# Kernel optimization log

Hardware: AMD Instinct MI355X
Metric: run time of the kernel (lower is better)

Reference implementation:

```python
import jax, jax.numpy as jnp
import numpy as np

THRESHOLD = 0.35      # overlap_thresh
NEGPOS_RATIO = 7
VAR0, VAR1 = 0.1, 0.2  # self.variance


def make_priors():
    # Standard RetinaFace 640x640 anchor grid -> 16800 priors (cx, cy, w, h)
    img = 640
    steps = [8, 16, 32]
    min_sizes = [[16, 32], [64, 128], [256, 512]]
    out = []
    for step, ms in zip(steps, min_sizes):
        f = img // step
        ii, jj = np.meshgrid(np.arange(f), np.arange(f), indexing="ij")
        cx = ((jj + 0.5) * step / img).ravel().astype(np.float32)
        cy = ((ii + 0.5) * step / img).ravel().astype(np.float32)
        for m in ms:
            s = np.full_like(cx, m / img)
            out.append(np.stack([cx, cy, s, s], axis=-1))
    return jnp.asarray(np.concatenate(out, axis=0), dtype=jnp.float32)


def jaccard(a, b):
    # a: [O,4] point-form gt boxes, b: [P,4] point-form priors -> IoU [O,P]
    lt = jnp.maximum(a[:, None, :2], b[None, :, :2])
    rb = jnp.minimum(a[:, None, 2:], b[None, :, 2:])
    wh = jnp.clip(rb - lt, 0.0)
    inter = wh[..., 0] * wh[..., 1]
    area_a = ((a[:, 2] - a[:, 0]) * (a[:, 3] - a[:, 1]))[:, None]
    area_b = ((b[:, 2] - b[:, 0]) * (b[:, 3] - b[:, 1]))[None, :]
    return inter / (area_a + area_b - inter)


def setup_inputs() -> dict:
    key = jax.random.key(0)
    ks = jax.random.split(key, 7)
    B, P, O = 64, 16800, 64
    loc_data = jax.random.normal(ks[0], (B, P, 4), jnp.float32)
    conf_data = jax.random.normal(ks[1], (B, P, 2), jnp.float32)
    landm_data = jax.random.normal(ks[2], (B, P, 10), jnp.float32)
    priors = make_priors()
    # targets: [B, O, 15] = [xmin ymin xmax ymax | 10 landmark coords | label]
    c = jax.random.uniform(ks[3], (B, O, 2), minval=0.15, maxval=0.85)
    wh = jax.random.uniform(ks[4], (B, O, 2), minval=0.05, maxval=0.3)
    boxes = jnp.concatenate([jnp.clip(c - wh / 2, 1e-3, 0.999),
                             jnp.clip(c + wh / 2, 1e-3, 0.999)], axis=-1)
    landms = jax.random.uniform(ks[5], (B, O, 10))
    lab = jnp.where(jax.random.uniform(ks[6], (B, O, 1)) < 0.8, 1.0, -1.0)
    targets = jnp.concatenate([boxes, landms, lab], axis=-1).astype(jnp.float32)
    return {"loc_data": loc_data, "conf_data": conf_data,
            "landm_data": landm_data, "priors": priors, "targets": targets}


def _smooth_l1(x):
    ax = jnp.abs(x)
    return jnp.where(ax < 1.0, 0.5 * ax * ax, ax - 0.5)


def reference(loc_data, conf_data, landm_data, priors, targets):
    B, P, C = conf_data.shape
    O = targets.shape[1]
    priors_pf = jnp.concatenate([priors[:, :2] - priors[:, 2:] * 0.5,
                                 priors[:, :2] + priors[:, 2:] * 0.5], axis=1)

    def match_one(t):
        truths = t[:, :4]
        landms = t[:, 4:14]
        labels = t[:, 14].astype(jnp.int32)
        ov = jaccard(truths, priors_pf)               # [O,P]
        bp_ov = ov.max(axis=1)                         # best prior per truth
        bp_idx = jnp.argmax(ov, axis=1)
        valid = bp_ov >= 0.2                           # RetinaFace gt filter
        bt_ov = ov.max(axis=0)                         # best truth per prior
        bt_idx = jnp.argmax(ov, axis=0)
        # index_fill_(best_prior_idx, 2) for valid gts, ensure best prior kept
        bt_ov = bt_ov.at[bp_idx].set(jnp.where(valid, 2.0, bt_ov[bp_idx]))
        bt_idx = bt_idx.at[bp_idx].set(jnp.arange(O))
        matched = truths[bt_idx]                       # [P,4] point form
        conf = labels[bt_idx]
        conf = jnp.where(bt_ov < THRESHOLD, 0, conf)
        # encode loc target
        g_cxcy = ((matched[:, :2] + matched[:, 2:]) * 0.5 - priors[:, :2]) / (VAR0 * priors[:, 2:])
        g_wh = jnp.log((matched[:, 2:] - matched[:, :2]) / priors[:, 2:]) / VAR1
        loc = jnp.concatenate([g_cxcy, g_wh], axis=1)
        # encode landmark target (5 points)
        ml = landms[bt_idx].reshape(P, 5, 2)
        lm = ((ml - priors[:, None, :2]) / (VAR0 * priors[:, None, 2:])).reshape(P, 10)
        any_valid = jnp.any(valid)                     # early-return branch of match()
        return (jnp.where(any_valid, loc, 0.0),
                jnp.where(any_valid, conf, 0),
                jnp.where(any_valid, lm, 0.0))

    loc_t, conf_t, landm_t = jax.vmap(match_one)(targets)
    loc_t = jax.lax.stop_gradient(loc_t)       # targets built from .data in torch
    landm_t = jax.lax.stop_gradient(landm_t)

    # landmark loss over conf_t > 0
    pos1 = conf_t > 0
    N1 = jnp.maximum(pos1.sum().astype(jnp.float32), 1.0)
    loss_landm = jnp.sum(jnp.where(pos1[..., None], _smooth_l1(landm_data - landm_t), 0.0))

    # localization loss over conf_t != 0 (labels -1 and 1 both positive)
    pos = conf_t != 0
    conf_t1 = jnp.where(pos, 1, conf_t)        # conf_t[pos] = 1 -> values in {0,1}
    loss_l = jnp.sum(jnp.where(pos[..., None], _smooth_l1(loc_data - loc_t), 0.0))

    # hard negative mining
    lse = jax.nn.logsumexp(conf_data, axis=2)                       # [B,P]
    picked = jnp.take_along_axis(conf_data, conf_t1[..., None], axis=2)[..., 0]
    ce_all = lse - picked                                            # per-anchor CE
    rank_score = jnp.where(pos, 0.0, ce_all)
    loss_idx = jnp.argsort(-rank_score, axis=1)
    idx_rank = jnp.argsort(loss_idx, axis=1)
    num_pos = pos.sum(axis=1, keepdims=True)
    num_neg = jnp.minimum(NEGPOS_RATIO * num_pos, P - 1)
    neg = idx_rank < num_neg
    union = pos | neg
    loss_c = jnp.sum(jnp.where(union, ce_all, 0.0))

    N = jnp.maximum(num_pos.sum().astype(jnp.float32), 1.0)
    return loss_l / N, loss_c / N, loss_landm / N1
```

## Files before the change

### kernel.cpp

```cpp
#include <hip/hip_runtime.h>
#include <math.h>

#define B 64
#define P 16800
#define O 64
#define THRESH 0.35f
#define VALID_T 0.2f
#define HB 2048
#define HSHIFT 21
#define MULT 2
#define CHB (MULT * 256)
#define NB2 ((P + CHB - 1) / CHB)
#define KD1B (B * NB2)
#define KB2B (B * O / 4)

__device__ __forceinline__ float smooth_l1(float x) {
    float ax = fabsf(x);
    return ax < 1.f ? 0.5f * ax * ax : ax - 0.5f;
}
__device__ __forceinline__ float lse2(float c0, float c1) {
    float m = fmaxf(c0, c1);
    return m + __logf(__expf(c0 - m) + __expf(c1 - m));
}
__device__ __forceinline__ void iou_upd(float4 t, float area_a,
                                        float px1, float py1, float px2, float py2,
                                        float area_b,
                                        float& bnum, float& bden, int& bio, int o) {
    float w = fmaxf(fminf(t.z, px2) - fmaxf(t.x, px1), 0.f);
    float h = fmaxf(fminf(t.w, py2) - fmaxf(t.y, py1), 0.f);
    float inter = w * h;
    float den = area_a + area_b - inter;
    if (inter * bden > bnum * den) { bnum = inter; bden = den; bio = o; }
}
__device__ __forceinline__ float wave_sum(float v) {
#pragma unroll
    for (int s = 32; s > 0; s >>= 1) v += __shfl_down(v, s, 64);
    return v;
}
__device__ __forceinline__ int wave_sum_i(int v) {
#pragma unroll
    for (int s = 32; s > 0; s >>= 1) v += __shfl_down(v, s, 64);
    return v;
}
__device__ __forceinline__ float wave_min(float v) {
#pragma unroll
    for (int s = 32; s > 0; s >>= 1) v = fminf(v, __shfl_xor(v, s, 64));
    return v;
}
__device__ __forceinline__ float wave_max(float v) {
#pragma unroll
    for (int s = 32; s > 0; s >>= 1) v = fmaxf(v, __shfl_xor(v, s, 64));
    return v;
}
__device__ __forceinline__ int wave_sufscan(int v, int lane) {
#pragma unroll
    for (int s = 1; s < 64; s <<= 1) {
        int o = __shfl_down(v, s, 64);
        if (lane + s < 64) v += o;
    }
    return v;
}

__global__ void __launch_bounds__(256) kMain(
        const float* __restrict__ loc_data, const float* __restrict__ conf_data,
        const float* __restrict__ landm_data, const float* __restrict__ priors,
        const float* __restrict__ targets,
        float* __restrict__ rank, int* __restrict__ hist,
        int* __restrict__ num_pos, float* __restrict__ pos_ce,
        float* __restrict__ gsum, int* __restrict__ np1_tot,
        unsigned long long* __restrict__ bp_final) {
    if (blockIdx.x >= KD1B) {
        int pair = (blockIdx.x - KD1B) * 4 + (threadIdx.x >> 6);
        int lane = threadIdx.x & 63;
        int o = pair & (O - 1);
        int b = pair >> 6;
        const float* tt = &targets[(b * O + o) * 15];
        float tx1 = tt[0], ty1 = tt[1], tx2 = tt[2], ty2 = tt[3];
        float area_a = (tx2 - tx1) * (ty2 - ty1);
        float4 tb = make_float4(tx1, ty1, tx2, ty2);
        float bn = 0.f, bd = 1.f;
        unsigned bp = 0u;
        const int fs[6]   = {80, 80, 40, 40, 20, 20};
        const int ms[6]   = {16, 32, 64, 128, 256, 512};
        const int base[6] = {0, 6400, 12800, 14400, 16000, 16400};
#pragma unroll
        for (int c = 0; c < 6; ++c) {
            int f = fs[c];
            float inv = (float)f;
            float h = (float)ms[c] * (0.5f / 640.f);
            int j0 = (int)floorf((tx1 - h) * inv - 0.5f) - 1; if (j0 < 0) j0 = 0;
            int j1 = (int)ceilf((tx2 + h) * inv - 0.5f) + 1;  if (j1 > f - 1) j1 = f - 1;
            int i0 = (int)floorf((ty1 - h) * inv - 0.5f) - 1; if (i0 < 0) i0 = 0;
            int i1 = (int)ceilf((ty2 + h) * inv - 0.5f) + 1;  if (i1 > f - 1) i1 = f - 1;
            if (j1 < j0 || i1 < i0) continue;
            int nj = j1 - j0 + 1;
            int n = (i1 - i0 + 1) * nj;
            float rcp_nj = 1.0f / (float)nj;
            for (int idx = lane; idx < n; idx += 64) {
                int ii = (int)((float)idx * rcp_nj);
                int jj = idx - ii * nj;
                if (jj < 0) { ii--; jj += nj; } else if (jj >= nj) { ii++; jj -= nj; }
                int p = base[c] + (i0 + ii) * f + (j0 + jj);
                float4 q = ((const float4*)priors)[p];
                float px1 = q.x - q.z * 0.5f, py1 = q.y - q.w * 0.5f;
                float px2 = q.x + q.z * 0.5f, py2 = q.y + q.w * 0.5f;
                float areab = (px2 - px1) * (py2 - py1);
                float w = fmaxf(fminf(tb.z, px2) - fmaxf(tb.x, px1), 0.f);
                float hh = fmaxf(fminf(tb.w, py2) - fmaxf(tb.y, py1), 0.f);
                float inter = w * hh;
                float den = area_a + areab - inter;
                float l = bn * den, r = inter * bd;
                if (r > l) { bn = inter; bd = den; bp = (unsigned)p; }
            }
        }
#pragma unroll
        for (int s = 32; s > 0; s >>= 1) {
            float no = __shfl_xor(bn, s, 64), dd = __shfl_xor(bd, s, 64);
            unsigned po = __shfl_xor(bp, s, 64);
            float l = bn * dd, r = no * bd;
            bool take = (r > l) || (r == l && po < bp);
            if (take) { bn = no; bd = dd; bp = po; }
        }
        if (lane == 0) {
            float iou = bn / bd;
            bp_final[b * O + o] = ((unsigned long long)__float_as_uint(iou) << 32)
                                | (unsigned)(0xFFFFFFFFu - bp);
        }
        return;
    }
    int blk = blockIdx.x % NB2;
    int b = blockIdx.x / NB2;
    int p0 = blk * CHB;
    __shared__ float4 t4[O];
    __shared__ float ta[O], lab[O];
    __shared__ float lm[O][10];
    __shared__ int lhist[HB];
    __shared__ float4 wbb[4];
    __shared__ int alist[O];
    __shared__ int s_cnt;
    __shared__ float wredf[3][4];
    __shared__ int wredi[2][4];
    int tid = threadIdx.x;
    if (tid < O) {
        const float* t = &targets[(b * O + tid) * 15];
        float a0 = t[0], a1 = t[1], a2 = t[2], a3 = t[3];
        t4[tid] = make_float4(a0, a1, a2, a3);
        ta[tid] = (a2 - a0) * (a3 - a1);
        lab[tid] = t[14];
    }
    for (int i = tid; i < O * 10; i += 256)
        lm[i / 10][i % 10] = targets[b * O * 15 + (i / 10) * 15 + 4 + (i % 10)];
    for (int i = tid; i < HB; i += 256) lhist[i] = 0;
    float px1[MULT], py1[MULT], px2[MULT], py2[MULT], areab[MULT];
    float4 pr4[MULT];
    float bnum[MULT], bden[MULT]; int bi[MULT]; bool act[MULT];
    float bx1 = 1e30f, by1 = 1e30f, bx2 = -1e30f, by2 = -1e30f;
#pragma unroll
    for (int mi = 0; mi < MULT; ++mi) {
        int p = p0 + mi * 256 + tid;
        act[mi] = (p < P);
        int pc = act[mi] ? p : (P - 1);
        float4 q = ((const float4*)priors)[pc];
        pr4[mi] = q;
        px1[mi] = q.x - q.z * 0.5f; py1[mi] = q.y - q.w * 0.5f;
        px2[mi] = q.x + q.z * 0.5f; py2[mi] = q.y + q.w * 0.5f;
        areab[mi] = (px2[mi] - px1[mi]) * (py2[mi] - py1[mi]);
        bx1 = fminf(bx1, px1[mi]); by1 = fminf(by1, py1[mi]);
        bx2 = fmaxf(bx2, px2[mi]); by2 = fmaxf(by2, py2[mi]);
        bnum[mi] = 0.f; bden[mi] = 1.f; bi[mi] = 0;
    }
    bx1 = wave_min(bx1); by1 = wave_min(by1);
    bx2 = wave_max(bx2); by2 = wave_max(by2);
    int wid = tid >> 6, lid = tid & 63;
    if (lid == 0) wbb[wid] = make_float4(bx1, by1, bx2, by2);
    __syncthreads();
    if (tid < 64) {
        float ux1 = fminf(fminf(wbb[0].x, wbb[1].x), fminf(wbb[2].x, wbb[3].x));
        float uy1 = fminf(fminf(wbb[0].y, wbb[1].y), fminf(wbb[2].y, wbb[3].y));
        float ux2 = fmaxf(fmaxf(wbb[0].z, wbb[1].z), fmaxf(wbb[2].z, wbb[3].z));
        float uy2 = fmaxf(fmaxf(wbb[0].w, wbb[1].w), fmaxf(wbb[2].w, wbb[3].w));
        float4 t = t4[tid];
        bool pass = (fminf(t.z, ux2) - fmaxf(t.x, ux1) > 0.f) &&
                    (fminf(t.w, uy2) - fmaxf(t.y, uy1) > 0.f);
        unsigned long long mask = __ballot(pass);
        if (tid == 0) s_cnt = __popcll(mask);
        if (pass) {
            int pos = __popcll(mask & ((1ull << tid) - 1ull));
            alist[pos] = tid;
        }
    }
    __syncthreads();
    int cnt = s_cnt;
    for (int li = 0; li < cnt; ++li) {
        int o = alist[li];
        float4 t = t4[o];
        float w0 = fminf(t.z, bx2) - fmaxf(t.x, bx1);
        float h0 = fminf(t.w, by2) - fmaxf(t.y, by1);
        if (w0 <= 0.f || h0 <= 0.f) continue;
        float area_a = ta[o];
#pragma unroll
        for (int mi = 0; mi < MULT; ++mi)
            iou_upd(t, area_a, px1[mi], py1[mi], px2[mi], py2[mi], areab[mi],
                    bnum[mi], bden[mi], bi[mi], o);
    }
    float ll = 0.f, llm = 0.f, cep = 0.f;
    int cp = 0, cp1 = 0;
#pragma unroll
    for (int mi = 0; mi < MULT; ++mi) {
        if (!act[mi]) continue;
        int p = p0 + mi * 256 + tid;
        float best = bnum[mi] / bden[mi];
        int conf = (best >= THRESH) ? (int)lab[bi[mi]] : 0;
        float2 c01 = ((const float2*)conf_data)[b * P + p];
        float c0 = c01.x, c1 = c01.y;
        float lse = lse2(c0, c1);
        bool pos = conf != 0;
        float ce = lse - (pos ? c1 : c0);
        float rv = pos ? 0.f : ce;
        rank[(size_t)b * P + p] = rv;
        atomicAdd(&lhist[__float_as_uint(rv) >> HSHIFT], 1);
        if (pos) {
            cp++; cep += ce;
            int ti = bi[mi];
            float cx = pr4[mi].x, cy = pr4[mi].y, sw = pr4[mi].z, sh = pr4[mi].w;
            float4 t = t4[ti];
            float gx = ((t.x + t.z) * 0.5f - cx) / (0.1f * sw);
            float gy = ((t.y + t.w) * 0.5f - cy) / (0.1f * sh);
            float gw = logf((t.z - t.x) / sw) / 0.2f;
            float gh = logf((t.w - t.y) / sh) / 0.2f;
            const float* ld = &loc_data[(size_t)(b * P + p) * 4];
            ll += smooth_l1(ld[0] - gx) + smooth_l1(ld[1] - gy) +
                  smooth_l1(ld[2] - gw) + smooth_l1(ld[3] - gh);
            if (conf > 0) {
                cp1++;
                const float* lmd = &landm_data[(size_t)(b * P + p) * 10];
                for (int k5 = 0; k5 < 5; ++k5) {
                    float lx = (lm[ti][k5 * 2 + 0] - cx) / (0.1f * sw);
                    float ly = (lm[ti][k5 * 2 + 1] - cy) / (0.1f * sh);
                    llm += smooth_l1(lmd[k5 * 2 + 0] - lx) + smooth_l1(lmd[k5 * 2 + 1] - ly);
                }
            }
        }
    }
    float s_ll = wave_sum(ll), s_llm = wave_sum(llm), s_cep = wave_sum(cep);
    int s_cp = wave_sum_i(cp), s_cp1 = wave_sum_i(cp1);
    if (lid == 0) {
        wredf[0][wid] = s_ll; wredf[1][wid] = s_llm; wredf[2][wid] = s_cep;
        wredi[0][wid] = s_cp; wredi[1][wid] = s_cp1;
    }
    __syncthreads();
    if (tid == 0) {
        float ll_t = wredf[0][0] + wredf[0][1] + wredf[0][2] + wredf[0][3];
        float llm_t = wredf[1][0] + wredf[1][1] + wredf[1][2] + wredf[1][3];
        float cep_t = wredf[2][0] + wredf[2][1] + wredf[2][2] + wredf[2][3];
        int cp_t = wredi[0][0] + wredi[0][1] + wredi[0][2] + wredi[0][3];
        int cp1_t = wredi[1][0] + wredi[1][1] + wredi[1][2] + wredi[1][3];
        if (ll_t != 0.f)  atomicAdd(&gsum[0], ll_t);
        if (llm_t != 0.f) atomicAdd(&gsum[1], llm_t);
        if (cep_t != 0.f) atomicAdd(&pos_ce[b], cep_t);
        if (cp_t)  atomicAdd(&num_pos[b], cp_t);
        if (cp1_t) atomicAdd(np1_tot, cp1_t);
    }
    int* gh = hist + (size_t)b * HB;
#pragma unroll
    for (int i = tid; i < HB; i += 256) {
        int c = lhist[i];
        if (c) atomicAdd(&gh[i], c);
    }
}

__global__ void __launch_bounds__(1024) kTail(
        const float* __restrict__ priors, const float* __restrict__ targets,
        const float* __restrict__ loc_data, const float* __restrict__ conf_data,
        const float* __restrict__ landm_data,
        const unsigned long long* __restrict__ bp_final,
        const float* __restrict__ rank, const int* __restrict__ hist,
        const int* __restrict__ num_pos, const float* __restrict__ pos_ce,
        float* __restrict__ gsum, int* __restrict__ np1_tot, int* __restrict__ np_tot,
        float* __restrict__ lossc_tot, int* __restrict__ done,
        float* __restrict__ out) {
    __shared__ __align__(16) unsigned lrow[P];
    __shared__ float4 t4[O];
    __shared__ float ta[O], lab[O];
    __shared__ int sp[O];
    __shared__ int lh[HB];
    __shared__ int chunkSum[256];
    __shared__ int suf[257];
    __shared__ int waveTot[4];
    __shared__ int hist2[256];
    __shared__ int s_np, s_bin0, s_kk0, s_bin, s_kk;
    __shared__ float wredf[16];
    __shared__ int wredi[16];
    __shared__ float s_sumgt;

    int b = blockIdx.x;
    int tid = threadIdx.x;
    const float* r = rank + (size_t)b * P;
    const float4* r4 = (const float4*)r;
    for (int i = tid; i < P / 4; i += 1024) {
        float4 q = r4[i];
        ((uint4*)lrow)[i] = make_uint4(__float_as_uint(q.x), __float_as_uint(q.y),
                                       __float_as_uint(q.z), __float_as_uint(q.w));
    }
    for (int i = tid; i < HB; i += 1024) lh[i] = hist[(size_t)b * HB + i];
    int p = 0, v = 0;
    if (tid < O) {
        const float* tt = &targets[(b * O + tid) * 15];
        float4 tj = make_float4(tt[0], tt[1], tt[2], tt[3]);
        t4[tid] = tj;
        ta[tid] = (tj.z - tj.x) * (tj.w - tj.y);
        lab[tid] = tt[14];
        unsigned long long kpk = bp_final[b * O + tid];
        p = (int)(0xFFFFFFFFu - (unsigned)(kpk & 0xFFFFFFFFu));
        float iou = __uint_as_float((unsigned)(kpk >> 32));
        v = (iou >= VALID_T) ? 1 : 0;
        sp[tid] = p;
    }
    __syncthreads();
    int dnp = 0, dn1 = 0;
    float dll = 0.f, dllm = 0.f, dce = 0.f;
    if (tid < O) {
        int j = tid;
        bool winner = true;
        for (int jj = j + 1; jj < O; ++jj)
            if (sp[jj] == p) { winner = false; break; }
        if (winner) {
            float4 q = ((const float4*)priors)[p];
            float px1 = q.x - q.z * 0.5f, py1 = q.y - q.w * 0.5f;
            float px2 = q.x + q.z * 0.5f, py2 = q.y + q.w * 0.5f;
            float areab = (px2 - px1) * (py2 - py1);
            float bnum = 0.f, bden = 1.f; int bi = 0;
            for (int o = 0; o < O; ++o)
                iou_upd(t4[o], ta[o], px1, py1, px2, py2, areab, bnum, bden, bi, o);
            float best = bnum / bden;
            float ov_new = v ? 2.0f : best;
            int conf_old = (best >= THRESH) ? (int)lab[bi] : 0;
            int conf_new = (ov_new >= THRESH) ? (int)lab[j] : 0;
            float2 c01 = ((const float2*)conf_data)[b * P + p];
            float c0 = c01.x, c1 = c01.y;
            float lse = lse2(c0, c1);
            bool po = conf_old != 0, pn = conf_new != 0;
            float ceo = lse - (po ? c1 : c0), cen = lse - (pn ? c1 : c0);
            float rvo = po ? 0.f : ceo, rvn = pn ? 0.f : cen;
            if (__float_as_uint(rvo) != __float_as_uint(rvn)) {
                lrow[p] = __float_as_uint(rvn);
                int bo = __float_as_uint(rvo) >> HSHIFT, bn = __float_as_uint(rvn) >> HSHIFT;
                if (bo != bn) { atomicAdd(&lh[bn], 1); atomicAdd(&lh[bo], -1); }
            }
            const float* ld = &loc_data[(size_t)(b * P + p) * 4];
            auto enc_ll = [&](int ti) -> float {
                float4 t = t4[ti];
                float gx = ((t.x + t.z) * 0.5f - q.x) / (0.1f * q.z);
                float gy = ((t.y + t.w) * 0.5f - q.y) / (0.1f * q.w);
                float gw = logf((t.z - t.x) / q.z) / 0.2f;
                float gh = logf((t.w - t.y) / q.w) / 0.2f;
                return smooth_l1(ld[0] - gx) + smooth_l1(ld[1] - gy) +
                       smooth_l1(ld[2] - gw) + smooth_l1(ld[3] - gh);
            };
            if (po) dll -= enc_ll(bi);
            if (pn) dll += enc_ll(j);
            dce = (pn ? cen : 0.f) - (po ? ceo : 0.f);
            dnp = (int)pn - (int)po;
            const float* lmd = &landm_data[(size_t)(b * P + p) * 10];
            auto enc_lm = [&](int ti) -> float {
                const float* lmt = &targets[(b * O + ti) * 15 + 4];
                float sum = 0.f;
                for (int k5 = 0; k5 < 5; ++k5) {
                    float lx = (lmt[k5 * 2 + 0] - q.x) / (0.1f * q.z);
                    float ly = (lmt[k5 * 2 + 1] - q.y) / (0.1f * q.w);
                    sum += smooth_l1(lmd[k5 * 2 + 0] - lx) + smooth_l1(lmd[k5 * 2 + 1] - ly);
                }
                return sum;
            };
            if (conf_old > 0) dllm -= enc_lm(bi);
            if (conf_new > 0) dllm += enc_lm(j);
            dn1 = (int)(conf_new > 0) - (int)(conf_old > 0);
        }
    }
    float pce_reg = 0.f;
    if (tid < 64) {
        float r_ll = wave_sum(dll), r_lm = wave_sum(dllm), r_ce = wave_sum(dce);
        int r_np = wave_sum_i(dnp), r_n1 = wave_sum_i(dn1);
        if (tid == 0) {
            if (r_ll != 0.f) atomicAdd(&gsum[0], r_ll);
            if (r_lm != 0.f) atomicAdd(&gsum[1], r_lm);
            pce_reg = pos_ce[b] + r_ce;
            int np = num_pos[b] + r_np;
            s_np = np;
            atomicAdd(np_tot, np);
            if (r_n1) atomicAdd(np1_tot, r_n1);
        }
    }
    __syncthreads();
    int k = s_np * 7;
    if (k > P - 1) k = P - 1;
    if (tid < 256) {
        int cs = 0;
#pragma unroll
        for (int i = 0; i < HB / 256; ++i) cs += lh[tid * (HB / 256) + i];
        chunkSum[tid] = cs;
    }
    if (tid == 0) { s_bin0 = (k <= 0) ? -1 : 0; s_kk0 = (k <= 0) ? 0 : k; }
    __syncthreads();
    {
        int lane = tid & 63;
        int vv = (tid < 256) ? chunkSum[tid] : 0;
        vv = wave_sufscan(vv, lane);
        if (tid < 256 && lane == 0) waveTot[tid >> 6] = vv;
        __syncthreads();
        if (tid < 256) {
            int after = 0;
            for (int g = (tid >> 6) + 1; g < 4; ++g) after += waveTot[g];
            suf[tid] = vv + after;
            if (tid == 0) suf[256] = 0;
        }
        __syncthreads();
        if (k > 0 && tid < 256) {
            if (suf[tid] >= k && suf[tid + 1] < k) {
                int cum = suf[tid + 1];
                for (int i = HB / 256 - 1; i >= 0; --i) {
                    int hv = lh[tid * (HB / 256) + i];
                    if (cum + hv >= k) { s_bin0 = tid * (HB / 256) + i; s_kk0 = k - cum; break; }
                    cum += hv;
                }
            }
        }
    }
    __syncthreads();
    int bin = s_bin0;
    int kk0 = s_kk0;
    float topk_b = 0.f;
    if (bin >= 0) {
        unsigned lo_bound = ((unsigned)(bin + 1)) << HSHIFT;
        float sumgt = 0.f;
        for (int pp = tid; pp < P; pp += 1024) {
            unsigned u = lrow[pp];
            if (u >= lo_bound) sumgt += __uint_as_float(u);
        }
        float sg = wave_sum(sumgt);
        if ((tid & 63) == 0) wredf[tid >> 6] = sg;
        __syncthreads();
        if (tid == 0) {
            float t = 0.f;
            for (int i = 0; i < 16; ++i) t += wredf[i];
            s_sumgt = t;
        }
        unsigned pref = ((unsigned)bin) << HSHIFT;
        unsigned resolved = 0xFFFFFFFFu << HSHIFT;
        int kk = kk0;
        const int shifts[3] = {13, 5, 0};
        const int nbins[3] = {256, 256, 32};
        for (int pass = 0; pass < 3; ++pass) {
            int sh = shifts[pass], nb = nbins[pass];
            if (tid < nb) hist2[tid] = 0;
            __syncthreads();
            for (int i = tid; i < P / 4; i += 1024) {
                uint4 u4 = ((const uint4*)lrow)[i];
                if ((u4.x & resolved) == pref) atomicAdd(&hist2[(u4.x >> sh) & (nb - 1)], 1);
                if ((u4.y & resolved) == pref) atomicAdd(&hist2[(u4.y >> sh) & (nb - 1)], 1);
                if ((u4.z & resolved) == pref) atomicAdd(&hist2[(u4.z >> sh) & (nb - 1)], 1);
                if ((u4.w & resolved) == pref) atomicAdd(&hist2[(u4.w >> sh) & (nb - 1)], 1);
            }
            __syncthreads();
            int lane = tid & 63;
            int vv = (tid < nb) ? hist2[tid] : 0;
            vv = wave_sufscan(vv, lane);
            if (tid < nb && lane == 0) waveTot[tid >> 6] = vv;
            __syncthreads();
            int ng = (nb + 63) >> 6;
            if (tid < nb) {
                int after = 0;
                for (int g = (tid >> 6) + 1; g < ng; ++g) after += waveTot[g];
                suf[tid] = vv + after;
                if (tid == 0) suf[nb] = 0;
            }
            __syncthreads();
            if (tid < nb) {
                if (suf[tid] >= kk && suf[tid + 1] < kk) { s_bin = tid; s_kk = kk - suf[tid + 1]; }
            }
            __syncthreads();
            pref |= ((unsigned)s_bin) << sh;
            resolved |= (unsigned)(nb - 1) << sh;
            kk = s_kk;
            __syncthreads();
        }
        float tv = __uint_as_float(pref);
        float sumS = 0.f; int cntS = 0;
        for (int pp = tid; pp < P; pp += 1024) {
            unsigned u = lrow[pp];
            if ((u >> HSHIFT) == (unsigned)bin) {
                float val = __uint_as_float(u);
                if (val > tv) { sumS += val; cntS++; }
            }
        }
        float s2 = wave_sum(sumS); int c2 = wave_sum_i(cntS);
        if ((tid & 63) == 0) { wredf[tid >> 6] = s2; wredi[tid >> 6] = c2; }
        __syncthreads();
        if (tid == 0) {
            float st = 0.f; int ct = 0;
            for (int i = 0; i < 16; ++i) { st += wredf[i]; ct += wredi[i]; }
            topk_b = s_sumgt + st + (float)(kk0 - ct) * tv;
        }
    }
    if (tid == 0) {
        atomicAdd(lossc_tot, pce_reg + topk_b);
        __threadfence();
        int old = atomicAdd(done, 1);
        if (old == B - 1) {
            float g0 = atomicAdd(&gsum[0], 0.f);
            float g1 = atomicAdd(&gsum[1], 0.f);
            float lc = atomicAdd(lossc_tot, 0.f);
            int np = atomicAdd(np_tot, 0);
            int n1 = atomicAdd(np1_tot, 0);
            float N = fmaxf((float)np, 1.f);
            float N1 = fmaxf((float)n1, 1.f);
            out[0] = g0 / N;
            out[1] = lc / N;
            out[2] = g1 / N1;
        }
    }
}

extern "C" void kernel_launch(void* const* d_in, const int* in_sizes, int n_in,
                              void* d_out, int out_size, void* d_ws, size_t ws_size,
                              hipStream_t stream) {
    const float* loc_data   = (const float*)d_in[0];
    const float* conf_data  = (const float*)d_in[1];
    const float* landm_data = (const float*)d_in[2];
    const float* priors     = (const float*)d_in[3];
    const float* targets    = (const float*)d_in[4];
    float* out = (float*)d_out;

    char* ws = (char*)d_ws;
    size_t off = 0;
    auto alloc = [&](size_t bytes) -> void* {
        void* pp = ws + off;
        off += (bytes + 255) & ~(size_t)255;
        return pp;
    };
    float* rank     = (float*)alloc((size_t)B * P * 4);
    unsigned long long* bp_final = (unsigned long long*)alloc((size_t)B * O * 8);
    size_t hist_bytes = (size_t)B * HB * 4;
    char* zbase = (char*)alloc(hist_bytes);
    int* hist = (int*)zbase;
    size_t acc_bytes = (size_t)(2 * B * 4 + 64);
    char* acc = (char*)alloc(acc_bytes);
    int*   num_pos      = (int*)acc;
    float* pos_ce       = (float*)(acc + B * 4);
    float* gsum         = (float*)(acc + 2 * B * 4);
    int*   np1_tot      = (int*)(acc + 2 * B * 4 + 8);
    int*   np_tot       = (int*)(acc + 2 * B * 4 + 12);
    float* lossc_tot    = (float*)(acc + 2 * B * 4 + 16);
    int*   done         = (int*)(acc + 2 * B * 4 + 20);
    size_t zlen = (size_t)((acc + acc_bytes) - zbase);

    hipMemsetAsync(zbase, 0, zlen, stream);
    kMain<<<dim3(KD1B + KB2B), dim3(256), 0, stream>>>(loc_data, conf_data, landm_data,
                                                       priors, targets, rank, hist,
                                                       num_pos, pos_ce, gsum, np1_tot,
                                                       bp_final);
    kTail<<<dim3(B), dim3(1024), 0, stream>>>(priors, targets, loc_data, conf_data,
                                              landm_data, bp_final, rank, hist,
                                              num_pos, pos_ce, gsum, np1_tot, np_tot,
                                              lossc_tot, done, out);
}
```

Measured before the change: 165.2 us.

## Prune IoU pairs by area ratio and build rank histogram in tail kernel

Adds an area-ratio bound that skips IoU evaluation for gt/prior pairs whose areas differ enough that IoU cannot reach the match threshold, both at block level and per prior. Moves the per-batch rank histogram construction from kMain (shared plus global atomics) into kTail, which counts from the rank row it already loads into shared memory. This removes the global histogram buffer, its memset and the global atomics, at the cost of extra shared atomics in the single-block-per-batch tail kernel.

```diff
diff --git a/kernel.cpp b/kernel.cpp
--- a/kernel.cpp
+++ b/kernel.cpp
@@ -8,6 +8,7 @@
 #define VALID_T 0.2f
 #define HB 2048
 #define HSHIFT 21
+#define AREA_M 0.34f
 #define MULT 2
 #define CHB (MULT * 256)
 #define NB2 ((P + CHB - 1) / CHB)
@@ -65,7 +66,7 @@
         const float* __restrict__ loc_data, const float* __restrict__ conf_data,
         const float* __restrict__ landm_data, const float* __restrict__ priors,
         const float* __restrict__ targets,
-        float* __restrict__ rank, int* __restrict__ hist,
+        float* __restrict__ rank,
         int* __restrict__ num_pos, float* __restrict__ pos_ce,
         float* __restrict__ gsum, int* __restrict__ np1_tot,
         unsigned long long* __restrict__ bp_final) {
@@ -134,8 +135,8 @@
     __shared__ float4 t4[O];
     __shared__ float ta[O], lab[O];
     __shared__ float lm[O][10];
-    __shared__ int lhist[HB];
     __shared__ float4 wbb[4];
+    __shared__ float2 wab[4];
     __shared__ int alist[O];
     __shared__ int s_cnt;
     __shared__ float wredf[3][4];
@@ -150,11 +151,11 @@
     }
     for (int i = tid; i < O * 10; i += 256)
         lm[i / 10][i % 10] = targets[b * O * 15 + (i / 10) * 15 + 4 + (i % 10)];
-    for (int i = tid; i < HB; i += 256) lhist[i] = 0;
     float px1[MULT], py1[MULT], px2[MULT], py2[MULT], areab[MULT];
     float4 pr4[MULT];
     float bnum[MULT], bden[MULT]; int bi[MULT]; bool act[MULT];
     float bx1 = 1e30f, by1 = 1e30f, bx2 = -1e30f, by2 = -1e30f;
+    float amn = 1e30f, amx = -1e30f;
 #pragma unroll
     for (int mi = 0; mi < MULT; ++mi) {
         int p = p0 + mi * 256 + tid;
@@ -167,21 +168,27 @@
         areab[mi] = (px2[mi] - px1[mi]) * (py2[mi] - py1[mi]);
         bx1 = fminf(bx1, px1[mi]); by1 = fminf(by1, py1[mi]);
         bx2 = fmaxf(bx2, px2[mi]); by2 = fmaxf(by2, py2[mi]);
+        amn = fminf(amn, areab[mi]); amx = fmaxf(amx, areab[mi]);
         bnum[mi] = 0.f; bden[mi] = 1.f; bi[mi] = 0;
     }
     bx1 = wave_min(bx1); by1 = wave_min(by1);
     bx2 = wave_max(bx2); by2 = wave_max(by2);
+    amn = wave_min(amn); amx = wave_max(amx);
     int wid = tid >> 6, lid = tid & 63;
-    if (lid == 0) wbb[wid] = make_float4(bx1, by1, bx2, by2);
+    if (lid == 0) { wbb[wid] = make_float4(bx1, by1, bx2, by2); wab[wid] = make_float2(amn, amx); }
     __syncthreads();
     if (tid < 64) {
         float ux1 = fminf(fminf(wbb[0].x, wbb[1].x), fminf(wbb[2].x, wbb[3].x));
         float uy1 = fminf(fminf(wbb[0].y, wbb[1].y), fminf(wbb[2].y, wbb[3].y));
         float ux2 = fmaxf(fmaxf(wbb[0].z, wbb[1].z), fmaxf(wbb[2].z, wbb[3].z));
         float uy2 = fmaxf(fmaxf(wbb[0].w, wbb[1].w), fmaxf(wbb[2].w, wbb[3].w));
+        float bmn = fminf(fminf(wab[0].x, wab[1].x), fminf(wab[2].x, wab[3].x));
+        float bmx = fmaxf(fmaxf(wab[0].y, wab[1].y), fmaxf(wab[2].y, wab[3].y));
         float4 t = t4[tid];
+        float Aa = ta[tid];
         bool pass = (fminf(t.z, ux2) - fmaxf(t.x, ux1) > 0.f) &&
-                    (fminf(t.w, uy2) - fmaxf(t.y, uy1) > 0.f);
+                    (fminf(t.w, uy2) - fmaxf(t.y, uy1) > 0.f) &&
+                    (Aa >= AREA_M * bmn) && (bmx >= AREA_M * Aa);
         unsigned long long mask = __ballot(pass);
         if (tid == 0) s_cnt = __popcll(mask);
         if (pass) {
@@ -197,11 +204,14 @@
         float w0 = fminf(t.z, bx2) - fmaxf(t.x, bx1);
         float h0 = fminf(t.w, by2) - fmaxf(t.y, by1);
         if (w0 <= 0.f || h0 <= 0.f) continue;
-        float area_a = ta[o];
-#pragma unroll
-        for (int mi = 0; mi < MULT; ++mi)
-            iou_upd(t, area_a, px1[mi], py1[mi], px2[mi], py2[mi], areab[mi],
-                    bnum[mi], bden[mi], bi[mi], o);
+        float Aa = ta[o];
+#pragma unroll
+        for (int mi = 0; mi < MULT; ++mi) {
+            float Ap = areab[mi];
+            if (Aa >= AREA_M * Ap && Ap >= AREA_M * Aa)
+                iou_upd(t, Aa, px1[mi], py1[mi], px2[mi], py2[mi], Ap,
+                        bnum[mi], bden[mi], bi[mi], o);
+        }
     }
     float ll = 0.f, llm = 0.f, cep = 0.f;
     int cp = 0, cp1 = 0;
@@ -218,7 +228,6 @@
         float ce = lse - (pos ? c1 : c0);
         float rv = pos ? 0.f : ce;
         rank[(size_t)b * P + p] = rv;
-        atomicAdd(&lhist[__float_as_uint(rv) >> HSHIFT], 1);
         if (pos) {
             cp++; cep += ce;
             int ti = bi[mi];
@@ -261,12 +270,6 @@
         if (cp_t)  atomicAdd(&num_pos[b], cp_t);
         if (cp1_t) atomicAdd(np1_tot, cp1_t);
     }
-    int* gh = hist + (size_t)b * HB;
-#pragma unroll
-    for (int i = tid; i < HB; i += 256) {
-        int c = lhist[i];
-        if (c) atomicAdd(&gh[i], c);
-    }
 }
 
 __global__ void __launch_bounds__(1024) kTail(
@@ -274,7 +277,7 @@
         const float* __restrict__ loc_data, const float* __restrict__ conf_data,
         const float* __restrict__ landm_data,
         const unsigned long long* __restrict__ bp_final,
-        const float* __restrict__ rank, const int* __restrict__ hist,
+        const float* __restrict__ rank,
         const int* __restrict__ num_pos, const float* __restrict__ pos_ce,
         float* __restrict__ gsum, int* __restrict__ np1_tot, int* __restrict__ np_tot,
         float* __restrict__ lossc_tot, int* __restrict__ done,
@@ -302,7 +305,7 @@
         ((uint4*)lrow)[i] = make_uint4(__float_as_uint(q.x), __float_as_uint(q.y),
                                        __float_as_uint(q.z), __float_as_uint(q.w));
     }
-    for (int i = tid; i < HB; i += 1024) lh[i] = hist[(size_t)b * HB + i];
+    for (int i = tid; i < HB; i += 1024) lh[i] = 0;
     int p = 0, v = 0;
     if (tid < O) {
         const float* tt = &targets[(b * O + tid) * 15];
@@ -316,6 +319,8 @@
         v = (iou >= VALID_T) ? 1 : 0;
         sp[tid] = p;
     }
+    __syncthreads();
+    for (int i = tid; i < P; i += 1024) atomicAdd(&lh[lrow[i] >> HSHIFT], 1);
     __syncthreads();
     int dnp = 0, dn1 = 0;
     float dll = 0.f, dllm = 0.f, dce = 0.f;
@@ -330,8 +335,11 @@
             float px2 = q.x + q.z * 0.5f, py2 = q.y + q.w * 0.5f;
             float areab = (px2 - px1) * (py2 - py1);
             float bnum = 0.f, bden = 1.f; int bi = 0;
-            for (int o = 0; o < O; ++o)
-                iou_upd(t4[o], ta[o], px1, py1, px2, py2, areab, bnum, bden, bi, o);
+            for (int o = 0; o < O; ++o) {
+                float Aa = ta[o];
+                if (Aa >= AREA_M * areab && areab >= AREA_M * Aa)
+                    iou_upd(t4[o], Aa, px1, py1, px2, py2, areab, bnum, bden, bi, o);
+            }
             float best = bnum / bden;
             float ov_new = v ? 2.0f : best;
             int conf_old = (best >= THRESH) ? (int)lab[bi] : 0;
@@ -540,9 +548,6 @@
     };
     float* rank     = (float*)alloc((size_t)B * P * 4);
     unsigned long long* bp_final = (unsigned long long*)alloc((size_t)B * O * 8);
-    size_t hist_bytes = (size_t)B * HB * 4;
-    char* zbase = (char*)alloc(hist_bytes);
-    int* hist = (int*)zbase;
     size_t acc_bytes = (size_t)(2 * B * 4 + 64);
     char* acc = (char*)alloc(acc_bytes);
     int*   num_pos      = (int*)acc;
@@ -552,15 +557,14 @@
     int*   np_tot       = (int*)(acc + 2 * B * 4 + 12);
     float* lossc_tot    = (float*)(acc + 2 * B * 4 + 16);
     int*   done         = (int*)(acc + 2 * B * 4 + 20);
-    size_t zlen = (size_t)((acc + acc_bytes) - zbase);
-
-    hipMemsetAsync(zbase, 0, zlen, stream);
+
+    hipMemsetAsync(acc, 0, acc_bytes, stream);
     kMain<<<dim3(KD1B + KB2B), dim3(256), 0, stream>>>(loc_data, conf_data, landm_data,
-                                                       priors, targets, rank, hist,
+                                                       priors, targets, rank,
                                                        num_pos, pos_ce, gsum, np1_tot,
                                                        bp_final);
     kTail<<<dim3(B), dim3(1024), 0, stream>>>(priors, targets, loc_data, conf_data,
-                                              landm_data, bp_final, rank, hist,
+                                              landm_data, bp_final, rank,
                                               num_pos, pos_ce, gsum, np1_tot, np_tot,
                                               lossc_tot, done, out);
 }
```

New measurement: 166.8 us. About the same (+1.0%).
